# Optimization experiments

Hardware: AMD Instinct MI355X
Metric: run time of the kernel (lower is better)

Reference implementation:

```python
import jax, jax.numpy as jnp
import numpy as np

EPS = 1e-15  # matches torch_geometric dense pooling EPS


def gcn_conv(x, src, dst, w, W, b, n):
    # GCNConv(normalize=False): linear first, then weighted scatter-add src->dst, then bias
    h = x @ W
    msg = w[:, None] * h[src]  # [E, out]
    return jax.ops.segment_sum(msg, dst, num_segments=n) + b


def setup_inputs() -> dict:
    key = jax.random.key(0)
    ks = jax.random.split(key, 8)
    N, E, d, k = 12288, 393216, 256, 16
    x = jax.random.normal(ks[0], (N, d), dtype=jnp.float32)
    edge_index = jax.random.randint(ks[1], (2, E), 0, N, dtype=jnp.int32)
    edge_weight = jax.random.uniform(ks[2], (E,), dtype=jnp.float32)
    sc = 1.0 / np.sqrt(d).astype(np.float32)
    W1 = jax.random.normal(ks[3], (d, d), dtype=jnp.float32) * sc
    b1 = jnp.zeros((d,), jnp.float32)
    W2 = jax.random.normal(ks[4], (d, d), dtype=jnp.float32) * sc
    b2 = jnp.zeros((d,), jnp.float32)
    Wm = jax.random.normal(ks[5], (d, k), dtype=jnp.float32) * sc
    bm = jnp.zeros((k,), jnp.float32)
    return dict(x=x, edge_weight=edge_weight, W1=W1, b1=b1, W2=W2, b2=b2,
                Wm=Wm, bm=bm, edge_index=edge_index)


def reference(x, edge_weight, W1, b1, W2, b2, Wm, bm, edge_index):
    src, dst = edge_index[0], edge_index[1]
    n = x.shape[0]
    # message-passing stack: GCNConv -> ReLU -> GCNConv -> ReLU
    h = jax.nn.relu(gcn_conv(x, src, dst, edge_weight, W1, b1, n))
    h = jax.nn.relu(gcn_conv(h, src, dst, edge_weight, W2, b2, n))
    # cluster MLP (single Linear, Identity activations)
    s_logits = h @ Wm + bm  # [N, k]
    # to_dense_adj(edge_index, edge_attr=edge_weight): dense [N, N]
    adj = jnp.zeros((n, n), x.dtype).at[src, dst].add(edge_weight)
    # just_balance_pool (batch of 1)
    s = jax.nn.softmax(s_logits, axis=-1)  # [N, k]
    out = s.T @ h              # pooled features (unused by module output)
    out_adj = s.T @ adj @ s    # pooled adjacency (unused by module output)
    gram = s.T @ s             # [k, k]
    k = s.shape[-1]
    b_loss = -jnp.trace(jnp.sqrt(gram + EPS)) / jnp.sqrt(jnp.float32(n * k))
    return s, b_loss
```

## Files before the change

kernel.cpp:

```cpp
#include <hip/hip_runtime.h>
#include <hip/hip_bf16.h>
#include <hip/hip_fp16.h>

#define D 256
#define KCL 16
#define EPS 1e-15f
#define PAD 128

typedef __attribute__((ext_vector_type(8))) short short8;
typedef __attribute__((ext_vector_type(4))) float f32x4;

__device__ inline short bfhi(float v) {
    __hip_bfloat16 b = __float2bfloat16(v);
    return __builtin_bit_cast(short, b);
}
__device__ inline float bf2f(short s) {
    __hip_bfloat16 b = __builtin_bit_cast(__hip_bfloat16, s);
    return __bfloat162float(b);
}

__global__ __launch_bounds__(256) void setup_k(const float* __restrict__ W1,
                                               const float* __restrict__ W2,
                                               short* __restrict__ Wt1h, short* __restrict__ Wt1l,
                                               short* __restrict__ Wt2h, short* __restrict__ Wt2l,
                                               const int* __restrict__ src,
                                               const int* __restrict__ dst,
                                               const float* __restrict__ ew,
                                               int* __restrict__ deg,
                                               int2* __restrict__ edges, int E) {
    int b = blockIdx.x;
    if (b < 512) {
        const float* W = (b < 256) ? W1 : W2;
        short* Th = (b < 256) ? Wt1h : Wt2h;
        short* Tl = (b < 256) ? Wt1l : Wt2l;
        int c = b & 255;
        int k = threadIdx.x;
        float v = W[(size_t)k * D + c];
        short h = bfhi(v);
        Th[(size_t)c * D + k] = h;
        Tl[(size_t)c * D + k] = bfhi(v - bf2f(h));
    } else {
        int e = (b - 512) * 256 + threadIdx.x;
        if (e < E) {
            int d = dst[e];
            int slot = atomicAdd(&deg[d], 1);
            if (slot < PAD)
                edges[(size_t)d * PAD + slot] = make_int2(src[e], __float_as_int(ew[e]));
        }
    }
}

#define GBM 64
#define GBK 32
#define APAD 40
__global__ __launch_bounds__(256) void gemm_k(const float* __restrict__ A,
                                              const short* __restrict__ Bth,
                                              const short* __restrict__ Btl,
                                              __half* __restrict__ C) {
    __shared__ short Ah[GBM][APAD];
    __shared__ short Al[GBM][APAD];
    int tid = threadIdx.x;
    int lane = tid & 63, w = tid >> 6;
    int bm = blockIdx.x * GBM, bn = blockIdx.y * 64;
    f32x4 acc[4];
#pragma unroll
    for (int i = 0; i < 4; ++i) acc[i] = (f32x4){0.f, 0.f, 0.f, 0.f};

    int r  = tid >> 2;
    int cc = (tid & 3) * 8;
    int ar = w * 16 + (lane & 15);
    int kq = (lane >> 4) * 8;

    for (int kk = 0; kk < D; kk += GBK) {
        const float* ap = &A[(size_t)(bm + r) * D + kk + cc];
        float4 v0 = *(const float4*)ap;
        float4 v1 = *(const float4*)(ap + 4);
        float vv[8] = {v0.x, v0.y, v0.z, v0.w, v1.x, v1.y, v1.z, v1.w};
        short8 hi, lo;
#pragma unroll
        for (int j = 0; j < 8; ++j) {
            short h = bfhi(vv[j]);
            hi[j] = h;
            lo[j] = bfhi(vv[j] - bf2f(h));
        }
        __syncthreads();
        *(short8*)&Ah[r][cc] = hi;
        *(short8*)&Al[r][cc] = lo;
        __syncthreads();

        short8 a_h = *(const short8*)&Ah[ar][kq];
        short8 a_l = *(const short8*)&Al[ar][kq];
#pragma unroll
        for (int nf = 0; nf < 4; ++nf) {
            int col = bn + nf * 16 + (lane & 15);
            short8 b_h = *(const short8*)&Bth[(size_t)col * D + kk + kq];
            short8 b_l = *(const short8*)&Btl[(size_t)col * D + kk + kq];
            acc[nf] = __builtin_amdgcn_mfma_f32_16x16x32_bf16(a_h, b_h, acc[nf], 0, 0, 0);
            acc[nf] = __builtin_amdgcn_mfma_f32_16x16x32_bf16(a_h, b_l, acc[nf], 0, 0, 0);
            acc[nf] = __builtin_amdgcn_mfma_f32_16x16x32_bf16(a_l, b_h, acc[nf], 0, 0, 0);
        }
    }
    int rbase = bm + w * 16 + (lane >> 4) * 4;
    int cb = bn + (lane & 15);
#pragma unroll
    for (int nf = 0; nf < 4; ++nf)
#pragma unroll
        for (int rr = 0; rr < 4; ++rr)
            C[(size_t)(rbase + rr) * D + cb + nf * 16] = __float2half(acc[nf][rr]);
}

__global__ __launch_bounds__(256) void spmm_k(const __half* __restrict__ h,
                                              const int2* __restrict__ edges,
                                              const int* __restrict__ deg,
                                              const float* __restrict__ bias,
                                              float* __restrict__ out) {
    int node = blockIdx.x;
    int t = threadIdx.x;
    int n = min(deg[node], PAD);
    __shared__ int   s_src[PAD];
    __shared__ float s_w[PAD];
    if (t < n) {
        int2 e = edges[(size_t)node * PAD + t];
        s_src[t] = e.x;
        s_w[t]   = __int_as_float(e.y);
    }
    __syncthreads();
    float acc = 0.f;
    int i = 0;
    for (; i + 4 <= n; i += 4) {
        float a0 = __half2float(h[(size_t)s_src[i]     * D + t]);
        float a1 = __half2float(h[(size_t)s_src[i + 1] * D + t]);
        float a2 = __half2float(h[(size_t)s_src[i + 2] * D + t]);
        float a3 = __half2float(h[(size_t)s_src[i + 3] * D + t]);
        acc = fmaf(s_w[i],     a0, acc);
        acc = fmaf(s_w[i + 1], a1, acc);
        acc = fmaf(s_w[i + 2], a2, acc);
        acc = fmaf(s_w[i + 3], a3, acc);
    }
    for (; i < n; ++i) acc = fmaf(s_w[i], __half2float(h[(size_t)s_src[i] * D + t]), acc);
    out[(size_t)node * D + t] = fmaxf(acc + bias[t], 0.f);
}

__global__ __launch_bounds__(256) void cluster_k(const float* __restrict__ h,
                                                 const float* __restrict__ Wm,
                                                 const float* __restrict__ bmv,
                                                 float* __restrict__ s_out) {
    int wave = threadIdx.x >> 6, lane = threadIdx.x & 63;
    int node = blockIdx.x * 4 + wave;
    float4 hv = *(const float4*)&h[(size_t)node * D + lane * 4];
    float p[KCL];
#pragma unroll
    for (int j = 0; j < KCL; ++j) p[j] = 0.f;
    const float* hp = (const float*)&hv;
#pragma unroll
    for (int u = 0; u < 4; ++u) {
        float hval = hp[u];
        const float4* wrow = (const float4*)&Wm[(size_t)(lane * 4 + u) * KCL];
#pragma unroll
        for (int q = 0; q < 4; ++q) {
            float4 wv = wrow[q];
            p[q * 4 + 0] = fmaf(hval, wv.x, p[q * 4 + 0]);
            p[q * 4 + 1] = fmaf(hval, wv.y, p[q * 4 + 1]);
            p[q * 4 + 2] = fmaf(hval, wv.z, p[q * 4 + 2]);
            p[q * 4 + 3] = fmaf(hval, wv.w, p[q * 4 + 3]);
        }
    }
#pragma unroll
    for (int off = 32; off; off >>= 1)
#pragma unroll
        for (int j = 0; j < KCL; ++j) p[j] += __shfl_xor(p[j], off, 64);
    if (lane == 0) {
        float mx = -1e30f;
#pragma unroll
        for (int j = 0; j < KCL; ++j) { p[j] += bmv[j]; mx = fmaxf(mx, p[j]); }
        float sum = 0.f;
#pragma unroll
        for (int j = 0; j < KCL; ++j) { p[j] = __expf(p[j] - mx); sum += p[j]; }
        float inv = 1.f / sum;
#pragma unroll
        for (int j = 0; j < KCL; ++j) s_out[(size_t)node * KCL + j] = p[j] * inv;
    }
}

__global__ __launch_bounds__(256) void sqloss_k(const float* __restrict__ s,
                                                float* __restrict__ diag,
                                                int* __restrict__ done,
                                                float* __restrict__ loss_out, int N) {
    int t = threadIdx.x;
    int j = t & 15;
    int g = t >> 4;
    float acc = 0.f;
    for (int i = blockIdx.x * 16 + g; i < N; i += gridDim.x * 16) {
        float v = s[(size_t)i * KCL + j];
        acc = fmaf(v, v, acc);
    }
    __shared__ float red[16][17];
    red[g][j] = acc;
    __syncthreads();
    if (g == 0) {
        float a = red[0][j];
#pragma unroll
        for (int gg = 1; gg < 16; ++gg) a += red[gg][j];
        atomicAdd(&diag[j], a);
    }
    __threadfence();
    __shared__ int lastFlag;
    if (t == 0) {
        int old = atomicAdd(done, 1);
        lastFlag = (old == (int)gridDim.x - 1);
    }
    __syncthreads();
    if (lastFlag && t == 0) {
        __threadfence();
        float sum = 0.f;
#pragma unroll
        for (int jj = 0; jj < KCL; ++jj) {
            float v = atomicAdd(&diag[jj], 0.f);
            sum += sqrtf(v + EPS);
        }
        loss_out[0] = -sum / sqrtf((float)N * (float)KCL);
    }
}

extern "C" void kernel_launch(void* const* d_in, const int* in_sizes, int n_in,
                              void* d_out, int out_size, void* d_ws, size_t ws_size,
                              hipStream_t stream) {
    const float* x  = (const float*)d_in[0];
    const float* ew = (const float*)d_in[1];
    const float* W1 = (const float*)d_in[2];
    const float* b1 = (const float*)d_in[3];
    const float* W2 = (const float*)d_in[4];
    const float* b2 = (const float*)d_in[5];
    const float* Wm = (const float*)d_in[6];
    const float* bm = (const float*)d_in[7];
    const int*   ei = (const int*)d_in[8];

    const int N = in_sizes[0] / D;
    const int E = in_sizes[1];
    const int* src = ei;
    const int* dst = ei + E;

    float* out = (float*)d_out;

    char* ws = (char*)d_ws;
    __half* G   = (__half*)ws;        ws += (size_t)N * D * 2;
    float* H      = (float*)ws;       ws += (size_t)N * D * 4;
    int*   deg    = (int*)ws;         ws += (size_t)N * 4;
    float* diag   = (float*)ws;       ws += 64;
    int*   done   = (int*)ws;         ws += 16;
    int2*  edges  = (int2*)ws;        ws += (size_t)N * PAD * 8;
    short* Wt1h   = (short*)ws;       ws += (size_t)D * D * 2;
    short* Wt1l   = (short*)ws;       ws += (size_t)D * D * 2;
    short* Wt2h   = (short*)ws;       ws += (size_t)D * D * 2;
    short* Wt2l   = (short*)ws;       ws += (size_t)D * D * 2;

    hipMemsetAsync(deg, 0, (size_t)N * 4 + 80, stream);
    int gE = (E + 255) / 256;
    setup_k<<<512 + gE, 256, 0, stream>>>(W1, W2, Wt1h, Wt1l, Wt2h, Wt2l,
                                          src, dst, ew, deg, edges, E);

    dim3 ggrid(N / GBM, 4);
    gemm_k<<<ggrid, 256, 0, stream>>>(x, Wt1h, Wt1l, G);
    spmm_k<<<N, 256, 0, stream>>>(G, edges, deg, b1, H);
    gemm_k<<<ggrid, 256, 0, stream>>>(H, Wt2h, Wt2l, G);
    spmm_k<<<N, 256, 0, stream>>>(G, edges, deg, b2, H);
    cluster_k<<<N / 4, 256, 0, stream>>>(H, Wm, bm, out);
    sqloss_k<<<64, 256, 0, stream>>>(out, diag, done, out + (size_t)N * KCL, N);
}
```

Baseline: 265.4 us.

## Vectorize SpMM to half2 with 128 threads and fuse balance loss into cluster kernel

The SpMM kernel now has each of 128 threads load a half2 pair per edge, packs edge src and weight into one int2 shared array, and writes float2 outputs. This halves the thread count per node and widens each gather. The separate sqloss kernel is removed: cluster_k writes softmax rows as float4, computes per-block squared sums into a partial buffer, and the last block reduces them to the loss. This saves one launch and one re-read of s, at the cost of a last-block serial reduction over N/4 partials.

```diff
diff --git a/kernel.cpp b/kernel.cpp
--- a/kernel.cpp
+++ b/kernel.cpp
@@ -10,11 +10,11 @@
 typedef __attribute__((ext_vector_type(8))) short short8;
 typedef __attribute__((ext_vector_type(4))) float f32x4;
 
-__device__ inline short bfhi(float v) {
+__device__ __forceinline__ short bfhi(float v) {
     __hip_bfloat16 b = __float2bfloat16(v);
     return __builtin_bit_cast(short, b);
 }
-__device__ inline float bf2f(short s) {
+__device__ __forceinline__ float bf2f(short s) {
     __hip_bfloat16 b = __builtin_bit_cast(__hip_bfloat16, s);
     return __bfloat162float(b);
 }
@@ -51,7 +51,6 @@
 }
 
 #define GBM 64
-#define GBK 32
 #define APAD 40
 __global__ __launch_bounds__(256) void gemm_k(const float* __restrict__ A,
                                               const short* __restrict__ Bth,
@@ -71,7 +70,7 @@
     int ar = w * 16 + (lane & 15);
     int kq = (lane >> 4) * 8;
 
-    for (int kk = 0; kk < D; kk += GBK) {
+    for (int kk = 0; kk < D; kk += 32) {
         const float* ap = &A[(size_t)(bm + r) * D + kk + cc];
         float4 v0 = *(const float4*)ap;
         float4 v1 = *(const float4*)(ap + 4);
@@ -109,7 +108,7 @@
             C[(size_t)(rbase + rr) * D + cb + nf * 16] = __float2half(acc[nf][rr]);
 }
 
-__global__ __launch_bounds__(256) void spmm_k(const __half* __restrict__ h,
+__global__ __launch_bounds__(128) void spmm_k(const __half* __restrict__ h,
                                               const int2* __restrict__ edges,
                                               const int* __restrict__ deg,
                                               const float* __restrict__ bias,
@@ -117,36 +116,51 @@
     int node = blockIdx.x;
     int t = threadIdx.x;
     int n = min(deg[node], PAD);
-    __shared__ int   s_src[PAD];
-    __shared__ float s_w[PAD];
-    if (t < n) {
-        int2 e = edges[(size_t)node * PAD + t];
-        s_src[t] = e.x;
-        s_w[t]   = __int_as_float(e.y);
-    }
-    __syncthreads();
-    float acc = 0.f;
+    __shared__ int2 se[PAD];
+    if (t < n) se[t] = edges[(size_t)node * PAD + t];
+    __syncthreads();
+    const __half2* h2 = (const __half2*)h;
+    float acc0 = 0.f, acc1 = 0.f;
     int i = 0;
     for (; i + 4 <= n; i += 4) {
-        float a0 = __half2float(h[(size_t)s_src[i]     * D + t]);
-        float a1 = __half2float(h[(size_t)s_src[i + 1] * D + t]);
-        float a2 = __half2float(h[(size_t)s_src[i + 2] * D + t]);
-        float a3 = __half2float(h[(size_t)s_src[i + 3] * D + t]);
-        acc = fmaf(s_w[i],     a0, acc);
-        acc = fmaf(s_w[i + 1], a1, acc);
-        acc = fmaf(s_w[i + 2], a2, acc);
-        acc = fmaf(s_w[i + 3], a3, acc);
-    }
-    for (; i < n; ++i) acc = fmaf(s_w[i], __half2float(h[(size_t)s_src[i] * D + t]), acc);
-    out[(size_t)node * D + t] = fmaxf(acc + bias[t], 0.f);
+        int2 e0 = se[i], e1 = se[i + 1], e2 = se[i + 2], e3 = se[i + 3];
+        float2 a0 = __half22float2(h2[(size_t)e0.x * (D / 2) + t]);
+        float2 a1 = __half22float2(h2[(size_t)e1.x * (D / 2) + t]);
+        float2 a2 = __half22float2(h2[(size_t)e2.x * (D / 2) + t]);
+        float2 a3 = __half22float2(h2[(size_t)e3.x * (D / 2) + t]);
+        float w0 = __int_as_float(e0.y), w1 = __int_as_float(e1.y);
+        float w2 = __int_as_float(e2.y), w3 = __int_as_float(e3.y);
+        acc0 = fmaf(w0, a0.x, acc0); acc1 = fmaf(w0, a0.y, acc1);
+        acc0 = fmaf(w1, a1.x, acc0); acc1 = fmaf(w1, a1.y, acc1);
+        acc0 = fmaf(w2, a2.x, acc0); acc1 = fmaf(w2, a2.y, acc1);
+        acc0 = fmaf(w3, a3.x, acc0); acc1 = fmaf(w3, a3.y, acc1);
+    }
+    for (; i < n; ++i) {
+        int2 e = se[i];
+        float2 a = __half22float2(h2[(size_t)e.x * (D / 2) + t]);
+        float wv = __int_as_float(e.y);
+        acc0 = fmaf(wv, a.x, acc0); acc1 = fmaf(wv, a.y, acc1);
+    }
+    float2 bv = *(const float2*)&bias[2 * t];
+    *(float2*)&out[(size_t)node * D + 2 * t] =
+        make_float2(fmaxf(acc0 + bv.x, 0.f), fmaxf(acc1 + bv.y, 0.f));
 }
 
 __global__ __launch_bounds__(256) void cluster_k(const float* __restrict__ h,
                                                  const float* __restrict__ Wm,
                                                  const float* __restrict__ bmv,
-                                                 float* __restrict__ s_out) {
-    int wave = threadIdx.x >> 6, lane = threadIdx.x & 63;
+                                                 float* __restrict__ s_out,
+                                                 float* __restrict__ partial,
+                                                 int* __restrict__ done,
+                                                 float* __restrict__ loss_out,
+                                                 int N) {
+    __shared__ float dssq[4][KCL];
+    __shared__ int lastFlag;
+    int tid = threadIdx.x;
+    int wave = tid >> 6, lane = tid & 63;
     int node = blockIdx.x * 4 + wave;
+    int nblk = N >> 2;
+
     float4 hv = *(const float4*)&h[(size_t)node * D + lane * 4];
     float p[KCL];
 #pragma unroll
@@ -177,48 +191,48 @@
 #pragma unroll
         for (int j = 0; j < KCL; ++j) { p[j] = __expf(p[j] - mx); sum += p[j]; }
         float inv = 1.f / sum;
-#pragma unroll
-        for (int j = 0; j < KCL; ++j) s_out[(size_t)node * KCL + j] = p[j] * inv;
-    }
-}
-
-__global__ __launch_bounds__(256) void sqloss_k(const float* __restrict__ s,
-                                                float* __restrict__ diag,
-                                                int* __restrict__ done,
-                                                float* __restrict__ loss_out, int N) {
-    int t = threadIdx.x;
-    int j = t & 15;
-    int g = t >> 4;
-    float acc = 0.f;
-    for (int i = blockIdx.x * 16 + g; i < N; i += gridDim.x * 16) {
-        float v = s[(size_t)i * KCL + j];
-        acc = fmaf(v, v, acc);
-    }
-    __shared__ float red[16][17];
-    red[g][j] = acc;
-    __syncthreads();
-    if (g == 0) {
-        float a = red[0][j];
-#pragma unroll
-        for (int gg = 1; gg < 16; ++gg) a += red[gg][j];
-        atomicAdd(&diag[j], a);
-    }
-    __threadfence();
-    __shared__ int lastFlag;
-    if (t == 0) {
-        int old = atomicAdd(done, 1);
-        lastFlag = (old == (int)gridDim.x - 1);
-    }
-    __syncthreads();
-    if (lastFlag && t == 0) {
+        float* so = &s_out[(size_t)node * KCL];
+#pragma unroll
+        for (int q = 0; q < 4; ++q) {
+            float s0 = p[q*4+0] * inv, s1 = p[q*4+1] * inv;
+            float s2 = p[q*4+2] * inv, s3 = p[q*4+3] * inv;
+            *(float4*)&so[q * 4] = make_float4(s0, s1, s2, s3);
+            dssq[wave][q*4+0] = s0 * s0; dssq[wave][q*4+1] = s1 * s1;
+            dssq[wave][q*4+2] = s2 * s2; dssq[wave][q*4+3] = s3 * s3;
+        }
+    }
+    __syncthreads();
+    if (tid < KCL)
+        partial[(size_t)blockIdx.x * KCL + tid] =
+            dssq[0][tid] + dssq[1][tid] + dssq[2][tid] + dssq[3][tid];
+    __syncthreads();
+
+    if (tid == 0) {
         __threadfence();
-        float sum = 0.f;
-#pragma unroll
-        for (int jj = 0; jj < KCL; ++jj) {
-            float v = atomicAdd(&diag[jj], 0.f);
-            sum += sqrtf(v + EPS);
-        }
-        loss_out[0] = -sum / sqrtf((float)N * (float)KCL);
+        int old = __hip_atomic_fetch_add(done, 1, __ATOMIC_ACQ_REL, __HIP_MEMORY_SCOPE_AGENT);
+        lastFlag = (old == nblk - 1) ? 1 : 0;
+    }
+    __syncthreads();
+    if (lastFlag) {
+        __threadfence();
+        int j = tid & 15, g = tid >> 4;
+        float acc = 0.f;
+        for (int rr = g; rr < nblk; rr += 16)
+            acc += __hip_atomic_load(&partial[(size_t)rr * KCL + j],
+                                     __ATOMIC_RELAXED, __HIP_MEMORY_SCOPE_AGENT);
+        __shared__ float red2[16][17];
+        red2[g][j] = acc;
+        __syncthreads();
+        if (tid == 0) {
+            float sum = 0.f;
+            for (int jj = 0; jj < KCL; ++jj) {
+                float v = 0.f;
+#pragma unroll
+                for (int gg = 0; gg < 16; ++gg) v += red2[gg][jj];
+                sum += sqrtf(v + EPS);
+            }
+            loss_out[0] = -sum / sqrtf((float)N * (float)KCL);
+        }
     }
 }
 
@@ -243,27 +257,27 @@
     float* out = (float*)d_out;
 
     char* ws = (char*)d_ws;
-    __half* G   = (__half*)ws;        ws += (size_t)N * D * 2;
-    float* H      = (float*)ws;       ws += (size_t)N * D * 4;
-    int*   deg    = (int*)ws;         ws += (size_t)N * 4;
-    float* diag   = (float*)ws;       ws += 64;
-    int*   done   = (int*)ws;         ws += 16;
-    int2*  edges  = (int2*)ws;        ws += (size_t)N * PAD * 8;
-    short* Wt1h   = (short*)ws;       ws += (size_t)D * D * 2;
-    short* Wt1l   = (short*)ws;       ws += (size_t)D * D * 2;
-    short* Wt2h   = (short*)ws;       ws += (size_t)D * D * 2;
-    short* Wt2l   = (short*)ws;       ws += (size_t)D * D * 2;
-
-    hipMemsetAsync(deg, 0, (size_t)N * 4 + 80, stream);
+    __half* G    = (__half*)ws;       ws += (size_t)N * D * 2;
+    float* H     = (float*)ws;        ws += (size_t)N * D * 4;
+    int*   deg   = (int*)ws;          ws += (size_t)N * 4;
+    int*   done  = (int*)ws;          ws += 64;
+    int2*  edges = (int2*)ws;         ws += (size_t)N * PAD * 8;
+    short* Wt1h  = (short*)ws;        ws += (size_t)D * D * 2;
+    short* Wt1l  = (short*)ws;        ws += (size_t)D * D * 2;
+    short* Wt2h  = (short*)ws;        ws += (size_t)D * D * 2;
+    short* Wt2l  = (short*)ws;        ws += (size_t)D * D * 2;
+    float* partial = (float*)ws;      ws += (size_t)(N / 4) * KCL * 4;
+
+    hipMemsetAsync(deg, 0, (size_t)N * 4 + 64, stream);
     int gE = (E + 255) / 256;
     setup_k<<<512 + gE, 256, 0, stream>>>(W1, W2, Wt1h, Wt1l, Wt2h, Wt2l,
                                           src, dst, ew, deg, edges, E);
 
     dim3 ggrid(N / GBM, 4);
     gemm_k<<<ggrid, 256, 0, stream>>>(x, Wt1h, Wt1l, G);
-    spmm_k<<<N, 256, 0, stream>>>(G, edges, deg, b1, H);
+    spmm_k<<<N, 128, 0, stream>>>(G, edges, deg, b1, H);
     gemm_k<<<ggrid, 256, 0, stream>>>(H, Wt2h, Wt2l, G);
-    spmm_k<<<N, 256, 0, stream>>>(G, edges, deg, b2, H);
-    cluster_k<<<N / 4, 256, 0, stream>>>(H, Wm, bm, out);
-    sqloss_k<<<64, 256, 0, stream>>>(out, diag, done, out + (size_t)N * KCL, N);
-}
+    spmm_k<<<N, 128, 0, stream>>>(G, edges, deg, b2, H);
+    cluster_k<<<N / 4, 256, 0, stream>>>(H, Wm, bm, out, partial, done,
+                                         out + (size_t)N * KCL, N);
+}
```

Result: slower. 393.8 us (+48.4%).
